# Performance work log

Measured on AMD Instinct MI355X. Metric: run time of the kernel, lower is better.

Reference implementation:

```python
import jax, jax.numpy as jnp
import numpy as np

B, T, C = 128, 256, 384
H, D = 6, 64

def setup_inputs() -> dict:
    key = jax.random.key(0)
    ks = jax.random.split(key, 6)
    s = 1.0 / np.sqrt(C)
    return {
        "x": jax.random.normal(ks[0], (B, T, C), dtype=jnp.float32),
        "Wq": jax.random.normal(ks[1], (H, C, D), dtype=jnp.float32) * s,
        "Wk": jax.random.normal(ks[2], (H, C, D), dtype=jnp.float32) * s,
        "Wv": jax.random.normal(ks[3], (H, C, D), dtype=jnp.float32) * s,
        "Wp": jax.random.normal(ks[4], (C, C), dtype=jnp.float32) * s,
        "bp": jnp.zeros((C,), dtype=jnp.float32),
    }

def reference(x, Wq, Wk, Wv, Wp, bp):
    # per-head projections (all heads at once): [B,T,C] x [H,C,D] -> [B,H,T,D]
    q = jnp.einsum("btc,hcd->bhtd", x, Wq)
    k = jnp.einsum("btc,hcd->bhtd", x, Wk)
    v = jnp.einsum("btc,hcd->bhtd", x, Wv)
    scale = 1.0 / jnp.sqrt(jnp.asarray(D, dtype=x.dtype))
    # scores [B,H,T,T], causal mask, softmax
    wei = jnp.einsum("bhqd,bhkd->bhqk", q, k) * scale
    causal = jnp.tril(jnp.ones((T, T), dtype=bool))
    wei = jnp.where(causal, wei, -jnp.inf)
    wei = jax.nn.softmax(wei, axis=-1)
    # dropout layers are identity in eval mode
    out = jnp.einsum("bhqk,bhkd->bhqd", wei, v)
    # concat heads: [B,T,H*D]
    out = out.transpose(0, 2, 1, 3).reshape(B, T, H * D)
    return out @ Wp + bp
```

## Files before the change

### kernel.cpp

```cpp
#include <hip/hip_runtime.h>
#include <stdint.h>


typedef __attribute__((ext_vector_type(8))) short bf16x8;
typedef __attribute__((ext_vector_type(4))) float f32x4;
typedef __attribute__((ext_vector_type(16))) float f32x16;

__device__ __forceinline__ unsigned short f2b(float f) {
    union { float f; unsigned int u; } v; v.f = f;
    unsigned int u = v.u + 0x7fffu + ((v.u >> 16) & 1u);
    return (unsigned short)(u >> 16);
}

__device__ __forceinline__ unsigned int pk2(float lo, float hi) {
    return (unsigned int)f2b(lo) | ((unsigned int)f2b(hi) << 16);
}

__device__ __forceinline__ void gload_lds16(const void* g, void* lds) {
    auto gp = reinterpret_cast<const __attribute__((address_space(1))) uint32_t*>(
        reinterpret_cast<uintptr_t>(g));
    auto lp = reinterpret_cast<__attribute__((address_space(3))) uint32_t*>(
        reinterpret_cast<uintptr_t>(lds));
    __builtin_amdgcn_global_load_lds(gp, lp, 16, 0, 0);
}

#define SBAR0() __builtin_amdgcn_sched_barrier(0)


__global__ void cvt_x_kernel(const float* __restrict__ x, unsigned short* __restrict__ xb, int n8) {
    int i = blockIdx.x * 256 + threadIdx.x;
    if (i >= n8) return;
    float4 a = ((const float4*)x)[(size_t)i * 2];
    float4 b = ((const float4*)x)[(size_t)i * 2 + 1];
    uint4 o;
    o.x = pk2(a.x, a.y); o.y = pk2(a.z, a.w);
    o.z = pk2(b.x, b.y); o.w = pk2(b.z, b.w);
    ((uint4*)xb)[i] = o;
}

__global__ void cvt_w_kernel(const float* __restrict__ Wq, const float* __restrict__ Wk,
                             const float* __restrict__ Wv, const float* __restrict__ Wp,
                             unsigned short* __restrict__ wt, unsigned short* __restrict__ wpt) {
    int i = blockIdx.x * 256 + threadIdx.x;
    if (i >= 589824) return;
    if (i < 442368) {
        int j = i / 384, c = i - j * 384;
        int p = j / 384, rem = j - p * 384;
        int h = rem >> 6, d = rem & 63;
        const float* W = (p == 0) ? Wq : ((p == 1) ? Wk : Wv);
        wt[i] = f2b(W[(size_t)(h * 384 + c) * 64 + d]);
    } else {
        int i2 = i - 442368;
        int n = i2 / 384, c = i2 - n * 384;
        wpt[i2] = f2b(Wp[(size_t)c * 384 + n]);
    }
}


__global__ __launch_bounds__(256, 3) void gemm_qkv(
    const unsigned short* __restrict__ xb,
    const unsigned short* __restrict__ wt,
    unsigned short* __restrict__ qO,
    unsigned short* __restrict__ kO,
    unsigned short* __restrict__ vO)
{
    extern __shared__ __align__(16) unsigned short smem[];
    unsigned short* AsBase = smem;
    unsigned short* BsBase = smem + 12288;

    const int tid  = threadIdx.x;
    const int lane = tid & 63;
    const int w    = tid >> 6;
    const int wm = w >> 1, wn = w & 1;

    const int flat = blockIdx.y * 9 + blockIdx.x;
    const int swz = (flat & 7) * 288 + (flat >> 3);
    const int bx = swz % 9, by = swz / 9;
    const int col0 = bx * 128;
    const int row0 = by * 128;

    const unsigned short* Abase = xb + (size_t)row0 * 384;
    const unsigned short* Bbase = wt + (size_t)col0 * 384;

    f32x4 acc[4][4];
#pragma unroll
    for (int mf = 0; mf < 4; ++mf)
#pragma unroll
        for (int nf = 0; nf < 4; ++nf)
#pragma unroll
            for (int r = 0; r < 4; ++r) acc[mf][nf][r] = 0.f;

    const int ci0 = tid;
    const int ci1 = tid + 256;
    const int r0c = ci0 >> 2, o0c = (ci0 & 3) ^ ((ci0 >> 3) & 3);
    const int r1c = ci1 >> 2, o1c = (ci1 & 3) ^ ((ci1 >> 3) & 3);
    const unsigned short* aSrc0 = Abase + (size_t)r0c * 384 + o0c * 8;
    const unsigned short* aSrc1 = Abase + (size_t)r1c * 384 + o1c * 8;
    const unsigned short* bSrc0 = Bbase + (size_t)r0c * 384 + o0c * 8;
    const unsigned short* bSrc1 = Bbase + (size_t)r1c * 384 + o1c * 8;
    const int cb = w * 64;

    auto STAGE = [&](int buf, int kt) {
        const int k0_ = kt * 32;
        gload_lds16(aSrc0 + k0_, AsBase + buf * 4096 + (cb + 0) * 8);
        gload_lds16(bSrc0 + k0_, BsBase + buf * 4096 + (cb + 0) * 8);
        gload_lds16(aSrc1 + k0_, AsBase + buf * 4096 + (cb + 256) * 8);
        gload_lds16(bSrc1 + k0_, BsBase + buf * 4096 + (cb + 256) * 8);
    };

    const int fr = lane & 15;
    const int oc = (lane >> 4) ^ ((fr >> 1) & 3);

    auto COMPUTE = [&](int buf) {
        const unsigned short* A = AsBase + buf * 4096;
        const unsigned short* B = BsBase + buf * 4096;
        bf16x8 aF[4], bF[4];
#pragma unroll
        for (int mf = 0; mf < 4; ++mf)
            aF[mf] = *(const bf16x8*)&A[(wm * 64 + mf * 16 + fr) * 32 + oc * 8];
#pragma unroll
        for (int nf = 0; nf < 4; ++nf)
            bF[nf] = *(const bf16x8*)&B[(wn * 64 + nf * 16 + fr) * 32 + oc * 8];
#pragma unroll
        for (int mf = 0; mf < 4; ++mf)
#pragma unroll
            for (int nf = 0; nf < 4; ++nf)
                acc[mf][nf] = __builtin_amdgcn_mfma_f32_16x16x32_bf16(aF[mf], bF[nf], acc[mf][nf], 0, 0, 0);
    };

    STAGE(0, 0);
    STAGE(1, 1);
    SBAR0();
    int bufS = 2, bufC = 0;
    for (int t = 0; t < 10; ++t) {
        STAGE(bufS, t + 2);
        bufS = (bufS == 2) ? 0 : bufS + 1;
        SBAR0();
        asm volatile("s_waitcnt vmcnt(8)" ::: "memory");
        SBAR0();
        __builtin_amdgcn_s_barrier();
        SBAR0();
        COMPUTE(bufC);
        bufC = (bufC == 2) ? 0 : bufC + 1;
        SBAR0();
        __builtin_amdgcn_s_barrier();
        SBAR0();
    }
    asm volatile("s_waitcnt vmcnt(4)" ::: "memory");
    SBAR0();
    __builtin_amdgcn_s_barrier();
    SBAR0();
    COMPUTE(1);
    SBAR0();
    __builtin_amdgcn_s_barrier();
    SBAR0();
    asm volatile("s_waitcnt vmcnt(0)" ::: "memory");
    SBAR0();
    __builtin_amdgcn_s_barrier();
    SBAR0();
    COMPUTE(2);
    __syncthreads();

    unsigned short* Ct = smem;
    const int co = tid & 15;
    const int rr = tid >> 4;
    const int colg = col0 + co * 8;
    const int p = colg / 384;
    const int rem = colg - p * 384;
    const int h = rem >> 6;
    const int d = rem & 63;
    unsigned short* dst = (p == 0) ? qO : ((p == 1) ? kO : vO);

#pragma unroll
    for (int ph = 0; ph < 2; ++ph) {
        if (wm == ph) {
#pragma unroll
            for (int mf = 0; mf < 4; ++mf)
#pragma unroll
                for (int nf = 0; nf < 4; ++nf)
#pragma unroll
                    for (int r = 0; r < 4; ++r)
                        Ct[(mf * 16 + (lane >> 4) * 4 + r) * 136 + wn * 64 + nf * 16 + (lane & 15)] =
                            f2b(acc[mf][nf][r]);
        }
        __syncthreads();
#pragma unroll
        for (int it = 0; it < 4; ++it) {
            const int r_loc = it * 16 + rr;
            const int m = row0 + ph * 64 + r_loc;
            const int b = m >> 8, t = m & 255;
            uint4 val = *(const uint4*)&Ct[r_loc * 136 + co * 8];
            *(uint4*)&dst[(size_t)((b * 6 + h) * 256 + t) * 64 + d] = val;
        }
        __syncthreads();
    }
}


__global__ __launch_bounds__(512, 4) void attn_kernel(
    const unsigned short* __restrict__ Qg,
    const unsigned short* __restrict__ Kg,
    const unsigned short* __restrict__ Vg,
    unsigned short* __restrict__ Og)
{
    extern __shared__ __align__(16) unsigned short asmem[];
    unsigned short* Ks = asmem;
    unsigned short* Vs = asmem + 256 * 72;
    unsigned short* Ot = asmem;
    const int bh = blockIdx.x;
    const int b = bh / 6, h = bh - b * 6;
    const int tid = threadIdx.x;
    const int lane = tid & 63;
    const int w = tid >> 6;
    const int lo = lane & 31, hi = lane >> 5;

    const unsigned short* kg = Kg + (size_t)bh * 256 * 64;
#pragma unroll
    for (int j = 0; j < 4; ++j) {
        int chunk = tid + 512 * j;
        int key = chunk >> 3, dc = (chunk & 7) * 8;
        *(uint4*)&Ks[key * 72 + dc] = *(const uint4*)&kg[key * 64 + dc];
    }
    {
        const unsigned short* vg = Vg + (size_t)bh * 256 * 64;
        uint32_t* Vs32 = (uint32_t*)Vs;
#pragma unroll
        for (int i = 0; i < 2; ++i) {
            int u = tid + 512 * i;
            int t2 = (u & 31) | ((u >> 8) << 5);
            int dm = (u >> 5) & 7;
            uint4 r0 = *(const uint4*)&vg[(2 * t2 + 0) * 64 + dm * 8];
            uint4 r1 = *(const uint4*)&vg[(2 * t2 + 1) * 64 + dm * 8];
            const unsigned short* e0 = (const unsigned short*)&r0;
            const unsigned short* e1 = (const unsigned short*)&r1;
#pragma unroll
            for (int j = 0; j < 8; ++j)
                Vs32[(dm * 8 + j) * 132 + t2] = (uint32_t)e0[j] | ((uint32_t)e1[j] << 16);
        }
    }
    __syncthreads();

    const int q0 = w * 32;
    const unsigned short* qg = Qg + (size_t)bh * 256 * 64 + (size_t)(q0 + lo) * 64 + hi * 8;
    bf16x8 qF[4];
#pragma unroll
    for (int dc = 0; dc < 4; ++dc) qF[dc] = *(const bf16x8*)(qg + dc * 16);

    float m = -1e30f, ssum = 0.f;
    f32x16 o0, o1;
#pragma unroll
    for (int r = 0; r < 16; ++r) { o0[r] = 0.f; o1[r] = 0.f; }

    for (int kt = 0; kt <= w; ++kt) {
        f32x16 s;
#pragma unroll
        for (int r = 0; r < 16; ++r) s[r] = 0.f;
#pragma unroll
        for (int dc = 0; dc < 4; ++dc) {
            bf16x8 aK = *(const bf16x8*)&Ks[(kt * 32 + lo) * 72 + dc * 16 + hi * 8];
            s = __builtin_amdgcn_mfma_f32_32x32x16_bf16(aK, qF[dc], s, 0, 0, 0);
        }
        float p[16];
        float pmax = -1e30f;
        const bool diag = (kt == w);
#pragma unroll
        for (int r = 0; r < 16; ++r) {
            float sv = s[r] * 0.125f;
            const int keyl = (r & 3) + 8 * (r >> 2) + 4 * hi;
            if (diag && keyl > lo) sv = -1e30f;
            p[r] = sv;
            pmax = fmaxf(pmax, sv);
        }
        pmax = fmaxf(pmax, __shfl_xor(pmax, 32, 64));
        const float mn = fmaxf(m, pmax);
        const float sf = __expf(m - mn);
        m = mn;
        ssum *= sf;
#pragma unroll
        for (int r = 0; r < 16; ++r) { o0[r] *= sf; o1[r] *= sf; }
        float rs = 0.f;
#pragma unroll
        for (int r = 0; r < 16; ++r) { p[r] = __expf(p[r] - m); rs += p[r]; }
        rs += __shfl_xor(rs, 32, 64);
        ssum += rs;

        union { unsigned short u[16]; bf16x8 v[2]; } P;
        {
            float recv[4];
#pragma unroll
            for (int j2 = 0; j2 < 4; ++j2) {
                float sendv = hi ? p[j2] : p[4 + j2];
                recv[j2] = __shfl_xor(sendv, 32, 64);
            }
#pragma unroll
            for (int i = 0; i < 4; ++i) P.u[i]     = f2b(hi ? recv[i] : p[i]);
#pragma unroll
            for (int i = 0; i < 4; ++i) P.u[4 + i] = f2b(hi ? p[4 + i] : recv[i]);
        }
        {
            float recv[4];
#pragma unroll
            for (int j2 = 0; j2 < 4; ++j2) {
                float sendv = hi ? p[8 + j2] : p[12 + j2];
                recv[j2] = __shfl_xor(sendv, 32, 64);
            }
#pragma unroll
            for (int i = 0; i < 4; ++i) P.u[8 + i]  = f2b(hi ? recv[i] : p[8 + i]);
#pragma unroll
            for (int i = 0; i < 4; ++i) P.u[12 + i] = f2b(hi ? p[12 + i] : recv[i]);
        }

#pragma unroll
        for (int kc = 0; kc < 2; ++kc) {
            bf16x8 aV0 = *(const bf16x8*)&Vs[lo * 264 + kt * 32 + kc * 16 + hi * 8];
            o0 = __builtin_amdgcn_mfma_f32_32x32x16_bf16(aV0, P.v[kc], o0, 0, 0, 0);
            bf16x8 aV1 = *(const bf16x8*)&Vs[(32 + lo) * 264 + kt * 32 + kc * 16 + hi * 8];
            o1 = __builtin_amdgcn_mfma_f32_32x32x16_bf16(aV1, P.v[kc], o1, 0, 0, 0);
        }
    }

    __syncthreads();
    const float inv = 1.f / ssum;
    {
        uint32_t* ot32 = (uint32_t*)&Ot[w * 32 * 72];
#pragma unroll
        for (int g = 0; g < 4; ++g) {
            const int dbase0 = 8 * g + 4 * hi;
            uint32_t w0 = pk2(o0[4 * g + 0] * inv, o0[4 * g + 1] * inv);
            uint32_t w1 = pk2(o0[4 * g + 2] * inv, o0[4 * g + 3] * inv);
            int dw = lo * 36 + (dbase0 >> 1);
            ot32[dw] = w0;
            ot32[dw + 1] = w1;
            uint32_t w2 = pk2(o1[4 * g + 0] * inv, o1[4 * g + 1] * inv);
            uint32_t w3 = pk2(o1[4 * g + 2] * inv, o1[4 * g + 3] * inv);
            int dw1 = lo * 36 + ((32 + dbase0) >> 1);
            ot32[dw1] = w2;
            ot32[dw1 + 1] = w3;
        }
    }
    __syncthreads();
    {
        const unsigned short* ot = &Ot[w * 32 * 72];
        const int q = lane >> 1;
        const int half = (lane & 1) * 32;
        unsigned short* og = Og + (size_t)(b * 256 + q0 + q) * 384 + h * 64 + half;
#pragma unroll
        for (int jj = 0; jj < 4; ++jj) {
            uint4 val = *(const uint4*)&ot[q * 72 + half + jj * 8];
            *(uint4*)&og[jj * 8] = val;
        }
    }
}


__global__ __launch_bounds__(256, 3) void gemm_proj(
    const unsigned short* __restrict__ ob,
    const unsigned short* __restrict__ wpt,
    const float* __restrict__ bp,
    float* __restrict__ out)
{
    __shared__ __align__(16) unsigned short As[3][128 * 32];
    __shared__ __align__(16) unsigned short Bs[3][128 * 32];
    const int tid  = threadIdx.x;
    const int lane = tid & 63;
    const int w    = tid >> 6;
    const int wm = w >> 1, wn = w & 1;

    const int flat = blockIdx.y * 3 + blockIdx.x;
    const int swz = (flat & 7) * 96 + (flat >> 3);
    const int bx = swz % 3, by = swz / 3;
    const int col0 = bx * 128;
    const int row0 = by * 128;

    const unsigned short* Abase = ob  + (size_t)row0 * 384;
    const unsigned short* Bbase = wpt + (size_t)col0 * 384;

    f32x4 acc[4][4];
#pragma unroll
    for (int mf = 0; mf < 4; ++mf)
#pragma unroll
        for (int nf = 0; nf < 4; ++nf)
#pragma unroll
            for (int r = 0; r < 4; ++r) acc[mf][nf][r] = 0.f;

    const int ci0 = tid;
    const int ci1 = tid + 256;
    const int r0c = ci0 >> 2, o0c = (ci0 & 3) ^ ((ci0 >> 3) & 3);
    const int r1c = ci1 >> 2, o1c = (ci1 & 3) ^ ((ci1 >> 3) & 3);
    const unsigned short* aSrc0 = Abase + (size_t)r0c * 384 + o0c * 8;
    const unsigned short* aSrc1 = Abase + (size_t)r1c * 384 + o1c * 8;
    const unsigned short* bSrc0 = Bbase + (size_t)r0c * 384 + o0c * 8;
    const unsigned short* bSrc1 = Bbase + (size_t)r1c * 384 + o1c * 8;
    const int cb = w * 64;

    auto STAGE = [&](int buf, int kt) {
        const int k0_ = kt * 32;
        gload_lds16(aSrc0 + k0_, (unsigned short*)As[buf] + (cb + 0) * 8);
        gload_lds16(bSrc0 + k0_, (unsigned short*)Bs[buf] + (cb + 0) * 8);
        gload_lds16(aSrc1 + k0_, (unsigned short*)As[buf] + (cb + 256) * 8);
        gload_lds16(bSrc1 + k0_, (unsigned short*)Bs[buf] + (cb + 256) * 8);
    };

    const int fr = lane & 15;
    const int oc = (lane >> 4) ^ ((fr >> 1) & 3);

    auto COMPUTE = [&](int buf) {
        const unsigned short* A = As[buf];
        const unsigned short* B = Bs[buf];
        bf16x8 aF[4], bF[4];
#pragma unroll
        for (int mf = 0; mf < 4; ++mf)
            aF[mf] = *(const bf16x8*)&A[(wm * 64 + mf * 16 + fr) * 32 + oc * 8];
#pragma unroll
        for (int nf = 0; nf < 4; ++nf)
            bF[nf] = *(const bf16x8*)&B[(wn * 64 + nf * 16 + fr) * 32 + oc * 8];
#pragma unroll
        for (int mf = 0; mf < 4; ++mf)
#pragma unroll
            for (int nf = 0; nf < 4; ++nf)
                acc[mf][nf] = __builtin_amdgcn_mfma_f32_16x16x32_bf16(aF[mf], bF[nf], acc[mf][nf], 0, 0, 0);
    };

    STAGE(0, 0);
    STAGE(1, 1);
    SBAR0();
    int bufS = 2, bufC = 0;
    for (int t = 0; t < 10; ++t) {
        STAGE(bufS, t + 2);
        bufS = (bufS == 2) ? 0 : bufS + 1;
        SBAR0();
        asm volatile("s_waitcnt vmcnt(8)" ::: "memory");
        SBAR0();
        __builtin_amdgcn_s_barrier();
        SBAR0();
        COMPUTE(bufC);
        bufC = (bufC == 2) ? 0 : bufC + 1;
        SBAR0();
        __builtin_amdgcn_s_barrier();
        SBAR0();
    }
    asm volatile("s_waitcnt vmcnt(4)" ::: "memory");
    SBAR0();
    __builtin_amdgcn_s_barrier();
    SBAR0();
    COMPUTE(1);
    SBAR0();
    __builtin_amdgcn_s_barrier();
    SBAR0();
    asm volatile("s_waitcnt vmcnt(0)" ::: "memory");
    SBAR0();
    __builtin_amdgcn_s_barrier();
    SBAR0();
    COMPUTE(2);

#pragma unroll
    for (int nf = 0; nf < 4; ++nf) {
        const int col = col0 + wn * 64 + nf * 16 + (lane & 15);
        const float bias = bp[col];
#pragma unroll
        for (int mf = 0; mf < 4; ++mf) {
            const int mbase = row0 + wm * 64 + mf * 16 + ((lane >> 4) * 4);
#pragma unroll
            for (int r = 0; r < 4; ++r) {
                const int mrow = mbase + r;
                out[(size_t)mrow * 384 + col] = acc[mf][nf][r] + bias;
            }
        }
    }
}


extern "C" void kernel_launch(void* const* d_in, const int* in_sizes, int n_in,
                              void* d_out, int out_size, void* d_ws, size_t ws_size,
                              hipStream_t stream) {
    const float* x  = (const float*)d_in[0];
    const float* Wq = (const float*)d_in[1];
    const float* Wk = (const float*)d_in[2];
    const float* Wv = (const float*)d_in[3];
    const float* Wp = (const float*)d_in[4];
    const float* bp = (const float*)d_in[5];
    float* out = (float*)d_out;

    char* ws = (char*)d_ws;
    unsigned short* xb  = (unsigned short*)(ws);
    unsigned short* qb  = (unsigned short*)(ws + 25165824);
    unsigned short* kb  = (unsigned short*)(ws + 50331648);
    unsigned short* vb  = (unsigned short*)(ws + 75497472);
    unsigned short* wt  = (unsigned short*)(ws + 100663296);
    unsigned short* wpt = (unsigned short*)(ws + 101548032);

    cvt_x_kernel<<<6144, 256, 0, stream>>>(x, xb, 1572864);
    cvt_w_kernel<<<2304, 256, 0, stream>>>(Wq, Wk, Wv, Wp, wt, wpt);
    gemm_qkv<<<dim3(9, 256), 256, 49152, stream>>>(xb, wt, qb, kb, vb);
    attn_kernel<<<768, 512, 70656, stream>>>(qb, kb, vb, xb);
    gemm_proj<<<dim3(3, 256), 256, 0, stream>>>(xb, wpt, bp, out);
}
```

Measured before the change: 109.8 us.

## Fuse fp32-to-bf16 conversion of x into QKV GEMM tile loads

Drops the separate cvt_x kernel. The QKV GEMM now streams fp32 x tiles into LDS with direct global-to-LDS loads and converts them to bf16 in registers using v_cvt_pk_bf16_f32 just before the MFMAs. This removes a full write and re-read of the bf16 copy of x plus one kernel launch. In exchange, the A-tile LDS footprint doubles to 72KB, occupancy drops from 3 to 2 blocks per CU, each of the 9 column blocks re-reads fp32 x, and the conversion ALU work is repeated in every block.

```diff
diff --git a/kernel.cpp b/kernel.cpp
--- a/kernel.cpp
+++ b/kernel.cpp
@@ -14,6 +14,12 @@
 
 __device__ __forceinline__ unsigned int pk2(float lo, float hi) {
     return (unsigned int)f2b(lo) | ((unsigned int)f2b(hi) << 16);
+}
+
+__device__ __forceinline__ uint32_t cvtpk(float lo, float hi) {
+    uint32_t r;
+    asm("v_cvt_pk_bf16_f32 %0, %1, %2" : "=v"(r) : "v"(lo), "v"(hi));
+    return r;
 }
 
 __device__ __forceinline__ void gload_lds16(const void* g, void* lds) {
@@ -26,17 +32,6 @@
 
 #define SBAR0() __builtin_amdgcn_sched_barrier(0)
 
-
-__global__ void cvt_x_kernel(const float* __restrict__ x, unsigned short* __restrict__ xb, int n8) {
-    int i = blockIdx.x * 256 + threadIdx.x;
-    if (i >= n8) return;
-    float4 a = ((const float4*)x)[(size_t)i * 2];
-    float4 b = ((const float4*)x)[(size_t)i * 2 + 1];
-    uint4 o;
-    o.x = pk2(a.x, a.y); o.y = pk2(a.z, a.w);
-    o.z = pk2(b.x, b.y); o.w = pk2(b.z, b.w);
-    ((uint4*)xb)[i] = o;
-}
 
 __global__ void cvt_w_kernel(const float* __restrict__ Wq, const float* __restrict__ Wk,
                              const float* __restrict__ Wv, const float* __restrict__ Wp,
@@ -57,16 +52,16 @@
 }
 
 
-__global__ __launch_bounds__(256, 3) void gemm_qkv(
-    const unsigned short* __restrict__ xb,
+__global__ __launch_bounds__(256, 2) void gemm_qkv(
+    const float* __restrict__ x,
     const unsigned short* __restrict__ wt,
     unsigned short* __restrict__ qO,
     unsigned short* __restrict__ kO,
     unsigned short* __restrict__ vO)
 {
     extern __shared__ __align__(16) unsigned short smem[];
-    unsigned short* AsBase = smem;
-    unsigned short* BsBase = smem + 12288;
+    float*          Af = (float*)smem;
+    unsigned short* Bf = smem + 24576;
 
     const int tid  = threadIdx.x;
     const int lane = tid & 63;
@@ -79,7 +74,7 @@
     const int col0 = bx * 128;
     const int row0 = by * 128;
 
-    const unsigned short* Abase = xb + (size_t)row0 * 384;
+    const float* Abase = x + (size_t)row0 * 384;
     const unsigned short* Bbase = wt + (size_t)col0 * 384;
 
     f32x4 acc[4][4];
@@ -90,37 +85,51 @@
 #pragma unroll
             for (int r = 0; r < 4; ++r) acc[mf][nf][r] = 0.f;
 
-    const int ci0 = tid;
-    const int ci1 = tid + 256;
-    const int r0c = ci0 >> 2, o0c = (ci0 & 3) ^ ((ci0 >> 3) & 3);
-    const int r1c = ci1 >> 2, o1c = (ci1 & 3) ^ ((ci1 >> 3) & 3);
-    const unsigned short* aSrc0 = Abase + (size_t)r0c * 384 + o0c * 8;
-    const unsigned short* aSrc1 = Abase + (size_t)r1c * 384 + o1c * 8;
-    const unsigned short* bSrc0 = Bbase + (size_t)r0c * 384 + o0c * 8;
-    const unsigned short* bSrc1 = Bbase + (size_t)r1c * 384 + o1c * 8;
+    const float* aSrc[4];
+#pragma unroll
+    for (int j = 0; j < 4; ++j) {
+        const int ci = tid + 256 * j;
+        aSrc[j] = Abase + (size_t)(ci >> 3) * 384 + ((ci & 7) ^ ((ci >> 3) & 7)) * 4;
+    }
+    const int bi0 = tid, bi1 = tid + 256;
+    const unsigned short* bSrc0 = Bbase + (size_t)(bi0 >> 2) * 384 + ((bi0 & 3) ^ ((bi0 >> 3) & 3)) * 8;
+    const unsigned short* bSrc1 = Bbase + (size_t)(bi1 >> 2) * 384 + ((bi1 & 3) ^ ((bi1 >> 3) & 3)) * 8;
     const int cb = w * 64;
 
     auto STAGE = [&](int buf, int kt) {
         const int k0_ = kt * 32;
-        gload_lds16(aSrc0 + k0_, AsBase + buf * 4096 + (cb + 0) * 8);
-        gload_lds16(bSrc0 + k0_, BsBase + buf * 4096 + (cb + 0) * 8);
-        gload_lds16(aSrc1 + k0_, AsBase + buf * 4096 + (cb + 256) * 8);
-        gload_lds16(bSrc1 + k0_, BsBase + buf * 4096 + (cb + 256) * 8);
+#pragma unroll
+        for (int j = 0; j < 4; ++j)
+            gload_lds16(aSrc[j] + k0_, Af + buf * 4096 + (cb + 256 * j) * 4);
+        gload_lds16(bSrc0 + k0_, Bf + buf * 4096 + (cb + 0) * 8);
+        gload_lds16(bSrc1 + k0_, Bf + buf * 4096 + (cb + 256) * 8);
     };
 
-    const int fr = lane & 15;
-    const int oc = (lane >> 4) ^ ((fr >> 1) & 3);
+    const int fr  = lane & 15;
+    const int oc  = lane >> 4;
+    const int qlA0 = (2 * oc)     ^ (fr & 7);
+    const int qlA1 = (2 * oc + 1) ^ (fr & 7);
+    const int ocB  = oc ^ ((fr >> 1) & 3);
 
     auto COMPUTE = [&](int buf) {
-        const unsigned short* A = AsBase + buf * 4096;
-        const unsigned short* B = BsBase + buf * 4096;
+        const float* A = Af + buf * 4096;
+        const unsigned short* B = Bf + buf * 4096;
         bf16x8 aF[4], bF[4];
 #pragma unroll
-        for (int mf = 0; mf < 4; ++mf)
-            aF[mf] = *(const bf16x8*)&A[(wm * 64 + mf * 16 + fr) * 32 + oc * 8];
+        for (int mf = 0; mf < 4; ++mf) {
+            const int rowA = wm * 64 + mf * 16 + fr;
+            f32x4 F0 = *(const f32x4*)&A[rowA * 32 + qlA0 * 4];
+            f32x4 F1 = *(const f32x4*)&A[rowA * 32 + qlA1 * 4];
+            union { uint32_t u[4]; bf16x8 v; } pk;
+            pk.u[0] = cvtpk(F0[0], F0[1]);
+            pk.u[1] = cvtpk(F0[2], F0[3]);
+            pk.u[2] = cvtpk(F1[0], F1[1]);
+            pk.u[3] = cvtpk(F1[2], F1[3]);
+            aF[mf] = pk.v;
+        }
 #pragma unroll
         for (int nf = 0; nf < 4; ++nf)
-            bF[nf] = *(const bf16x8*)&B[(wn * 64 + nf * 16 + fr) * 32 + oc * 8];
+            bF[nf] = *(const bf16x8*)&B[(wn * 64 + nf * 16 + fr) * 32 + ocB * 8];
 #pragma unroll
         for (int mf = 0; mf < 4; ++mf)
 #pragma unroll
@@ -136,7 +145,7 @@
         STAGE(bufS, t + 2);
         bufS = (bufS == 2) ? 0 : bufS + 1;
         SBAR0();
-        asm volatile("s_waitcnt vmcnt(8)" ::: "memory");
+        asm volatile("s_waitcnt vmcnt(12)" ::: "memory");
         SBAR0();
         __builtin_amdgcn_s_barrier();
         SBAR0();
@@ -146,7 +155,7 @@
         __builtin_amdgcn_s_barrier();
         SBAR0();
     }
-    asm volatile("s_waitcnt vmcnt(4)" ::: "memory");
+    asm volatile("s_waitcnt vmcnt(6)" ::: "memory");
     SBAR0();
     __builtin_amdgcn_s_barrier();
     SBAR0();
@@ -482,16 +491,15 @@
     float* out = (float*)d_out;
 
     char* ws = (char*)d_ws;
-    unsigned short* xb  = (unsigned short*)(ws);
+    unsigned short* ob  = (unsigned short*)(ws);
     unsigned short* qb  = (unsigned short*)(ws + 25165824);
     unsigned short* kb  = (unsigned short*)(ws + 50331648);
     unsigned short* vb  = (unsigned short*)(ws + 75497472);
     unsigned short* wt  = (unsigned short*)(ws + 100663296);
     unsigned short* wpt = (unsigned short*)(ws + 101548032);
 
-    cvt_x_kernel<<<6144, 256, 0, stream>>>(x, xb, 1572864);
     cvt_w_kernel<<<2304, 256, 0, stream>>>(Wq, Wk, Wv, Wp, wt, wpt);
-    gemm_qkv<<<dim3(9, 256), 256, 49152, stream>>>(xb, wt, qb, kb, vb);
-    attn_kernel<<<768, 512, 70656, stream>>>(qb, kb, vb, xb);
-    gemm_proj<<<dim3(3, 256), 256, 0, stream>>>(xb, wpt, bp, out);
-}
+    gemm_qkv<<<dim3(9, 256), 256, 73728, stream>>>(x, wt, qb, kb, vb);
+    attn_kernel<<<768, 512, 70656, stream>>>(qb, kb, vb, ob);
+    gemm_proj<<<dim3(3, 256), 256, 0, stream>>>(ob, wpt, bp, out);
+}
```

After: 109.6 us. No clear change (-0.2%).
